# Optimization experiments

Hardware: AMD Instinct MI355X
Metric: run time of the kernel (lower is better)

The kernel has to match this reference:

```python
import jax, jax.numpy as jnp
import numpy as np

N = 20000
NEG_SLOPE = 0.2


def gat_conv(x, src, dst, W, att_src, att_dst, bias, heads, ch, concat):
    # x: [N, F_in]; src/dst: [E] (messages flow src -> dst, softmax grouped by dst)
    n = x.shape[0]
    h = (x @ W).reshape(n, heads, ch)                      # [N, H, C]
    a_s = jnp.sum(h * att_src, axis=-1)                    # [N, H]
    a_d = jnp.sum(h * att_dst, axis=-1)                    # [N, H]
    e = jax.nn.leaky_relu(a_s[src] + a_d[dst], NEG_SLOPE)  # [E, H]
    m = jax.ops.segment_max(e, dst, num_segments=n)        # segment-softmax (stable)
    ex = jnp.exp(e - m[dst])
    denom = jax.ops.segment_sum(ex, dst, num_segments=n)
    alpha = ex / (denom[dst] + 1e-16)                      # [E, H]
    msg = h[src] * alpha[:, :, None]                       # [E, H, C]
    out = jax.ops.segment_sum(msg, dst, num_segments=n)    # [N, H, C]
    out = out.reshape(n, heads * ch) if concat else out.mean(axis=1)
    return out + bias


def setup_inputs() -> dict:
    key = jax.random.key(0)
    ks = jax.random.split(key, 24)
    in_ch, h_ch, out_ch, H, OH = 512, 128, 64, 4, 6
    hid = H * h_ch  # 512
    s = 0.1
    d = {
        "x": jax.random.normal(ks[0], (N, in_ch), jnp.float32),
        "edge_index": jax.random.randint(ks[1], (2, 160000), 0, N, jnp.int32),
        "W1": jax.random.normal(ks[2], (in_ch, H * h_ch), jnp.float32) * s,
        "as1": jax.random.normal(ks[3], (1, H, h_ch), jnp.float32) * s,
        "ad1": jax.random.normal(ks[4], (1, H, h_ch), jnp.float32) * s,
        "b1": jnp.zeros((H * h_ch,), jnp.float32),
        "lW1": jax.random.normal(ks[5], (in_ch, hid), jnp.float32) * s,
        "lb1": jnp.zeros((hid,), jnp.float32),
        "W2": jax.random.normal(ks[6], (hid, H * h_ch), jnp.float32) * s,
        "as2": jax.random.normal(ks[7], (1, H, h_ch), jnp.float32) * s,
        "ad2": jax.random.normal(ks[8], (1, H, h_ch), jnp.float32) * s,
        "b2": jnp.zeros((H * h_ch,), jnp.float32),
        "lW2": jax.random.normal(ks[9], (hid, hid), jnp.float32) * s,
        "lb2": jnp.zeros((hid,), jnp.float32),
        "W3": jax.random.normal(ks[10], (hid, OH * out_ch), jnp.float32) * s,
        "as3": jax.random.normal(ks[11], (1, OH, out_ch), jnp.float32) * s,
        "ad3": jax.random.normal(ks[12], (1, OH, out_ch), jnp.float32) * s,
        "b3": jnp.zeros((out_ch,), jnp.float32),
        "lW3": jax.random.normal(ks[13], (hid, out_ch), jnp.float32) * s,
        "lb3": jnp.zeros((out_ch,), jnp.float32),
    }
    return d


def reference(x, edge_index, W1, as1, ad1, b1, lW1, lb1,
              W2, as2, ad2, b2, lW2, lb2,
              W3, as3, ad3, b3, lW3, lb3):
    n = x.shape[0]
    loops = jnp.arange(n, dtype=edge_index.dtype)  # PyG GATConv add_self_loops=True
    src = jnp.concatenate([edge_index[0], loops])
    dst = jnp.concatenate([edge_index[1], loops])
    h = jax.nn.elu(gat_conv(x, src, dst, W1, as1, ad1, b1, 4, 128, True) + x @ lW1 + lb1)
    h = jax.nn.elu(gat_conv(h, src, dst, W2, as2, ad2, b2, 4, 128, True) + h @ lW2 + lb2)
    out = gat_conv(h, src, dst, W3, as3, ad3, b3, 6, 64, False) + h @ lW3 + lb3
    return out
```

## Files before the change

kernel.cpp:

```cpp
#include <hip/hip_runtime.h>
#include <cstddef>
#include <cstdint>
#include <type_traits>

#define N_NODES 20000
#define NPAD 20096
#define E0_EDGES 160000
#define E_TOT (E0_EDGES + N_NODES)
#define CAP 64

typedef __bf16 bf16x8 __attribute__((ext_vector_type(8)));
typedef float f32x4 __attribute__((ext_vector_type(4)));
typedef ushort ushort8 __attribute__((ext_vector_type(8)));

__device__ __forceinline__ ushort f2bf(float f) {
  uint32_t u = __float_as_uint(f);
  return (ushort)((u + 0x7FFFu + ((u >> 16) & 1u)) >> 16);
}
__device__ __forceinline__ float bf2f(ushort h) {
  return __uint_as_float((uint32_t)h << 16);
}

__device__ __forceinline__ int SW(int r) { return ((r >> 1) & 3) ^ ((r >> 3) & 1); }

#define GLOAD16(g, l)                                                         \
  __builtin_amdgcn_global_load_lds(                                           \
      (const __attribute__((address_space(1))) void*)(uintptr_t)(g),          \
      (__attribute__((address_space(3))) void*)(uint32_t)(uintptr_t)(l),      \
      16, 0, 0)


__global__ void fill_csr_kernel(const int* __restrict__ ei, int* __restrict__ cnt,
                                int* __restrict__ slots) {
  int e = blockIdx.x * blockDim.x + threadIdx.x;
  if (e >= E_TOT) return;
  int src, dst;
  if (e < E0_EDGES) { src = ei[e]; dst = ei[E0_EDGES + e]; }
  else              { src = e - E0_EDGES; dst = src; }
  int pos = atomicAdd(&cnt[dst], 1);
  if (pos < CAP) slots[dst * CAP + pos] = src;
}


__global__ void convert_x_kernel(const float* __restrict__ x, ushort* __restrict__ xb) {
  size_t i = ((size_t)blockIdx.x * blockDim.x + threadIdx.x) * 4;
  if (i >= (size_t)NPAD * 512) return;
  if (i < (size_t)N_NODES * 512) {
    float4 v = *(const float4*)(x + i);
    ushort4 o;
    o.x = f2bf(v.x); o.y = f2bf(v.y); o.z = f2bf(v.z); o.w = f2bf(v.w);
    *(ushort4*)(xb + i) = o;
  } else {
    *(ushort4*)(xb + i) = make_ushort4(0, 0, 0, 0);
  }
}

__global__ void transpose_all_kernel(
    const float* __restrict__ W1, const float* __restrict__ lW1,
    const float* __restrict__ W2, const float* __restrict__ lW2,
    const float* __restrict__ W3, const float* __restrict__ lW3,
    ushort* __restrict__ Bt1, ushort* __restrict__ Bt2, ushort* __restrict__ Bt3) {
  __shared__ float tile[32][33];
  const int K = 512;
  int z = blockIdx.z;
  const float* W; ushort* B; int M;
  switch (z) {
    case 0:  W = W1;  B = Bt1;              M = 512; break;
    case 1:  W = lW1; B = Bt1 + 512 * 512;  M = 512; break;
    case 2:  W = W2;  B = Bt2;              M = 512; break;
    case 3:  W = lW2; B = Bt2 + 512 * 512;  M = 512; break;
    case 4:  W = W3;  B = Bt3;              M = 384; break;
    default: W = lW3; B = Bt3 + 384 * 512;  M = 64;  break;
  }
  int mb = blockIdx.x * 32, kb = blockIdx.y * 32;
  if (mb >= M) return;
  int tx = threadIdx.x, ty = threadIdx.y;
#pragma unroll
  for (int i = 0; i < 32; i += 8)
    tile[ty + i][tx] = W[(size_t)(kb + ty + i) * M + mb + tx];
  __syncthreads();
#pragma unroll
  for (int i = 0; i < 32; i += 8)
    B[(size_t)(mb + ty + i) * K + kb + tx] = f2bf(tile[tx][ty + i]);
}


template <typename Out1T>
__global__ __launch_bounds__(512, 6) void mfma_gemm_kernel(
    const ushort* __restrict__ A,
    const ushort* __restrict__ Bt,
    ushort* __restrict__ out0, int ld0, int split,
    Out1T* __restrict__ out1, int ld1, int Mout1, const float* __restrict__ bias1,
    const float* __restrict__ att_sw, const float* __restrict__ att_dw,
    float* __restrict__ a_sp, float* __restrict__ a_dp,
    int nheads, int headC,
    int NT, int nwg) {
  const int K = 512;
  __shared__ __attribute__((aligned(16))) ushort As[3][128][32];
  __shared__ __attribute__((aligned(16))) ushort Bs[3][128][32];

  int tid = threadIdx.x, lane = tid & 63, wave = tid >> 6;
  int wrow = (wave >> 1) * 32, wcol = (wave & 1) * 64;

  size_t K2 = (size_t)K * 2;
  int rofs = lane >> 2;
  int gch = (lane & 3) ^ SW(rofs);
  int srow = wave * 16;

  int fr = lane & 15, hi = lane >> 4;
  int rch = hi ^ SW(fr);

  char* AsB = (char*)&As[0][0][0];
  char* BsB = (char*)&Bs[0][0][0];

  int q = nwg >> 3, r = nwg & 7;

  for (int w0 = blockIdx.x; w0 < nwg; w0 += gridDim.x) {
    int xcd = w0 & 7, pos = w0 >> 3;
    int wgid = (xcd < r ? xcd * (q + 1) : r * (q + 1) + (xcd - r) * q) + pos;
    int by = wgid / NT, bx = wgid - by * NT;
    int bm = by * 128, bn = bx * 128;

    const char* pA = (const char*)A + (size_t)(bm + srow + rofs) * K2 + gch * 16;
    const char* pB = (const char*)Bt + (size_t)(bn + srow + rofs) * K2 + gch * 16;

    f32x4 acc[2][4] = {};

#pragma unroll
    for (int s = 0; s < 2; ++s) {
      GLOAD16(pA, AsB + s * 8192 + srow * 64);
      GLOAD16(pB, BsB + s * 8192 + srow * 64);
      pA += 64; pB += 64;
    }

    for (int k = 0; k < 16; ++k) {
      if (k + 1 < 16) asm volatile("s_waitcnt vmcnt(2) lgkmcnt(0)" ::: "memory");
      else            asm volatile("s_waitcnt vmcnt(0) lgkmcnt(0)" ::: "memory");
      __builtin_amdgcn_s_barrier();
      asm volatile("" ::: "memory");
      if (k + 2 < 16) {
        int ss = (k + 2) % 3;
        GLOAD16(pA, AsB + ss * 8192 + srow * 64);
        GLOAD16(pB, BsB + ss * 8192 + srow * 64);
        pA += 64; pB += 64;
      }
      {
        int sc = k % 3;
        bf16x8 af[2], bf[4];
#pragma unroll
        for (int i = 0; i < 2; ++i)
          af[i] = *(const bf16x8*)&As[sc][wrow + i * 16 + fr][rch * 8];
#pragma unroll
        for (int j = 0; j < 4; ++j)
          bf[j] = *(const bf16x8*)&Bs[sc][wcol + j * 16 + fr][rch * 8];
#pragma unroll
        for (int i = 0; i < 2; ++i)
#pragma unroll
          for (int j = 0; j < 4; ++j)
            acc[i][j] = __builtin_amdgcn_mfma_f32_16x16x32_bf16(af[i], bf[j], acc[i][j], 0, 0, 0);
      }
      asm volatile("" ::: "memory");
    }

    asm volatile("s_waitcnt lgkmcnt(0)" ::: "memory");
    __builtin_amdgcn_s_barrier();
    asm volatile("" ::: "memory");

    int colg = bn + wcol;
    bool lower = colg < split;
    int g4 = hi << 2;
    int ccol = fr;
#pragma unroll
    for (int i = 0; i < 2; ++i) {
#pragma unroll
      for (int rr = 0; rr < 4; ++rr) {
        int row = bm + wrow + g4 + i * 16 + rr;
        if (row >= N_NODES) continue;
#pragma unroll
        for (int j = 0; j < 4; ++j) {
          int col = colg + j * 16 + ccol;
          float v = acc[i][j][rr];
          if (lower) {
            out0[(size_t)row * ld0 + col] = f2bf(v);
          } else {
            int c1 = col - split;
            if (c1 < Mout1) {
              float b = v + bias1[c1];
              if constexpr (std::is_same<Out1T, ushort>::value)
                out1[(size_t)row * ld1 + c1] = f2bf(b);
              else
                out1[(size_t)row * ld1 + c1] = b;
            }
          }
        }
      }
    }

    if (lower) {
      int hd = colg / headC;
      int cb = colg - hd * headC;
      int half = (cb >> 6) & 1;
      float ws4[4], wd4[4];
#pragma unroll
      for (int j = 0; j < 4; ++j) {
        int cc = hd * headC + cb + j * 16 + ccol;
        ws4[j] = att_sw[cc];
        wd4[j] = att_dw[cc];
      }
#pragma unroll
      for (int i = 0; i < 2; ++i) {
#pragma unroll
        for (int rr = 0; rr < 4; ++rr) {
          float ps = 0.f, pd = 0.f;
#pragma unroll
          for (int j = 0; j < 4; ++j) { ps += acc[i][j][rr] * ws4[j]; pd += acc[i][j][rr] * wd4[j]; }
#pragma unroll
          for (int o = 1; o < 16; o <<= 1) { ps += __shfl_xor(ps, o); pd += __shfl_xor(pd, o); }
          if ((lane & 15) == 0) {
            int row = bm + wrow + g4 + i * 16 + rr;
            if (row < N_NODES) {
              size_t idx = ((size_t)row * nheads + hd) * 2;
              if (headC == 128) {
                a_sp[idx + half] = ps;
                a_dp[idx + half] = pd;
              } else {
                a_sp[idx] = ps;  a_sp[idx + 1] = 0.f;
                a_dp[idx] = pd;  a_dp[idx + 1] = 0.f;
              }
            }
          }
        }
      }
    }
  }
}


template <int H, int C>
__global__ __launch_bounds__(256) void gather12_fused(
    const int* __restrict__ cnt, const int* __restrict__ slots,
    const float* __restrict__ a_sp, const float* __restrict__ a_dp,
    const ushort* __restrict__ hbuf, const float* __restrict__ gat_bias,
    const ushort* __restrict__ skip_in, ushort* __restrict__ outbuf) {
  __shared__ float al[H][CAP];
  __shared__ int srcs[CAP];
  __shared__ float part[4][H * C];
  int n = blockIdx.x;
  int t = threadIdx.x, lane = t & 63, w = t >> 6;
  int deg = min(cnt[n], CAP);

  int sj = 0;
  if (lane < deg) sj = slots[n * CAP + lane];
  {
    int hd = w;
    float e = -1e30f;
    if (lane < deg) {
      size_t is = ((size_t)sj * H + hd) * 2;
      size_t id = ((size_t)n * H + hd) * 2;
      float v = a_sp[is] + a_sp[is + 1] + a_dp[id] + a_dp[id + 1];
      e = v > 0.f ? v : 0.2f * v;
    }
    float m = e;
#pragma unroll
    for (int o = 32; o > 0; o >>= 1) m = fmaxf(m, __shfl_xor(m, o));
    float ex = (lane < deg) ? expf(e - m) : 0.f;
    float s = ex;
#pragma unroll
    for (int o = 32; o > 0; o >>= 1) s += __shfl_xor(s, o);
    float inv = 1.f / (s + 1e-16f);
    if (lane < deg) al[hd][lane] = ex * inv;
  }
  if (w == 0 && lane < deg) srcs[lane] = sj;
  __syncthreads();

  int f0 = 8 * lane, hd = lane >> 4;
  float a8[8] = {};
  for (int j = w; j < deg; j += 4) {
    float a = al[hd][j];
    ushort8 hv = *(const ushort8*)(hbuf + (size_t)srcs[j] * (H * C) + f0);
#pragma unroll
    for (int e = 0; e < 8; ++e) a8[e] += a * bf2f(hv[e]);
  }
  *(f32x4*)&part[w][f0] = *(f32x4*)&a8[0];
  *(f32x4*)&part[w][f0 + 4] = *(f32x4*)&a8[4];
  __syncthreads();

  int g0 = 2 * t;
  float s0 = part[0][g0] + part[1][g0] + part[2][g0] + part[3][g0];
  float s1 = part[0][g0 + 1] + part[1][g0 + 1] + part[2][g0 + 1] + part[3][g0 + 1];
  uint32_t sk = *(const uint32_t*)(skip_in + (size_t)n * (H * C) + g0);
  float o0 = s0 + gat_bias[g0 + 0] + bf2f((ushort)(sk & 0xffffu));
  float o1 = s1 + gat_bias[g0 + 1] + bf2f((ushort)(sk >> 16));
  o0 = o0 > 0.f ? o0 : (expf(o0) - 1.f);
  o1 = o1 > 0.f ? o1 : (expf(o1) - 1.f);
  uint32_t ov = (uint32_t)f2bf(o0) | ((uint32_t)f2bf(o1) << 16);
  *(uint32_t*)(outbuf + (size_t)n * (H * C) + g0) = ov;
}


__global__ __launch_bounds__(128) void gather3_fused(
    const int* __restrict__ cnt, const int* __restrict__ slots,
    const float* __restrict__ a_sp, const float* __restrict__ a_dp,
    const ushort* __restrict__ hbuf , const float* __restrict__ b3,
    float* __restrict__ out ) {
  __shared__ float al[6][CAP];
  __shared__ int srcs[CAP];
  __shared__ float part[6][64];
  int n = blockIdx.x;
  int t = threadIdx.x, lane = t & 63, w = t >> 6;
  int deg = min(cnt[n], CAP);

  int sj = 0;
  if (lane < deg) sj = slots[n * CAP + lane];
#pragma unroll
  for (int hh = 0; hh < 3; ++hh) {
    int hd = 3 * w + hh;
    float e = -1e30f;
    if (lane < deg) {
      size_t is = ((size_t)sj * 6 + hd) * 2;
      size_t id = ((size_t)n * 6 + hd) * 2;
      float v = a_sp[is] + a_sp[is + 1] + a_dp[id] + a_dp[id + 1];
      e = v > 0.f ? v : 0.2f * v;
    }
    float m = e;
#pragma unroll
    for (int o = 32; o > 0; o >>= 1) m = fmaxf(m, __shfl_xor(m, o));
    float ex = (lane < deg) ? expf(e - m) : 0.f;
    float s = ex;
#pragma unroll
    for (int o = 32; o > 0; o >>= 1) s += __shfl_xor(s, o);
    float inv = (1.f / 6.f) / (s + 1e-16f);
    if (lane < deg) al[hd][lane] = ex * inv;
  }
  if (w == 0 && lane < deg) srcs[lane] = sj;
  __syncthreads();

  if (t < 96) {
    int hd = t >> 4, c4 = (t & 15) * 4;
    float a4[4] = {};
    for (int j = 0; j < deg; ++j) {
      float a = al[hd][j];
      ushort4 hv = *(const ushort4*)(hbuf + (size_t)srcs[j] * 384 + hd * 64 + c4);
      a4[0] += a * bf2f(hv.x);
      a4[1] += a * bf2f(hv.y);
      a4[2] += a * bf2f(hv.z);
      a4[3] += a * bf2f(hv.w);
    }
    *(f32x4*)&part[hd][c4] = *(f32x4*)&a4[0];
  }
  __syncthreads();
  if (t < 64) {
    float s = part[0][t] + part[1][t] + part[2][t] +
              part[3][t] + part[4][t] + part[5][t];
    size_t oi = (size_t)n * 64 + t;
    out[oi] += s + b3[t];
  }
}


extern "C" void kernel_launch(void* const* d_in, const int* in_sizes, int n_in,
                              void* d_out, int out_size, void* d_ws, size_t ws_size,
                              hipStream_t stream) {
  const float* x   = (const float*)d_in[0];
  const int*   ei  = (const int*)d_in[1];
  const float* W1  = (const float*)d_in[2];
  const float* as1 = (const float*)d_in[3];
  const float* ad1 = (const float*)d_in[4];
  const float* b1  = (const float*)d_in[5];
  const float* lW1 = (const float*)d_in[6];
  const float* lb1 = (const float*)d_in[7];
  const float* W2  = (const float*)d_in[8];
  const float* as2 = (const float*)d_in[9];
  const float* ad2 = (const float*)d_in[10];
  const float* b2  = (const float*)d_in[11];
  const float* lW2 = (const float*)d_in[12];
  const float* lb2 = (const float*)d_in[13];
  const float* W3  = (const float*)d_in[14];
  const float* as3 = (const float*)d_in[15];
  const float* ad3 = (const float*)d_in[16];
  const float* b3  = (const float*)d_in[17];
  const float* lW3 = (const float*)d_in[18];
  const float* lb3 = (const float*)d_in[19];
  float* out = (float*)d_out;

  char* ws = (char*)d_ws;
  auto alloc = [&](size_t bytes) -> void* {
    void* p = (void*)ws;
    ws += (bytes + 255) & ~(size_t)255;
    return p;
  };
  ushort* xb    = (ushort*)alloc((size_t)NPAD * 512 * 2);
  ushort* Pb    = (ushort*)alloc((size_t)NPAD * 512 * 2);
  ushort* Qb    = (ushort*)alloc((size_t)NPAD * 512 * 2);
  ushort* skipb = (ushort*)alloc((size_t)N_NODES * 512 * 2);
  ushort* hb    = (ushort*)alloc((size_t)N_NODES * 512 * 2);
  ushort* Bt1   = (ushort*)alloc((size_t)1024 * 512 * 2);
  ushort* Bt2   = (ushort*)alloc((size_t)1024 * 512 * 2);
  ushort* Bt3   = (ushort*)alloc((size_t)512 * 512 * 2);
  float*  a_sp  = (float*)alloc((size_t)N_NODES * 6 * 2 * 4);
  float*  a_dp  = (float*)alloc((size_t)N_NODES * 6 * 2 * 4);
  int*    cnt   = (int*)alloc((size_t)N_NODES * 4);
  int*    slots = (int*)alloc((size_t)N_NODES * CAP * 4);

  hipMemsetAsync(cnt, 0, N_NODES * sizeof(int), stream);
  fill_csr_kernel<<<(E_TOT + 255) / 256, 256, 0, stream>>>(ei, cnt, slots);

  convert_x_kernel<<<((NPAD * 512 / 4) + 255) / 256, 256, 0, stream>>>(x, xb);
  transpose_all_kernel<<<dim3(16, 16, 6), dim3(32, 8), 0, stream>>>(
      W1, lW1, W2, lW2, W3, lW3, Bt1, Bt2, Bt3);

  const int NBY = NPAD / 128;
  const int NWG12 = NBY * 8;
  const int NWG3  = NBY * 4;
  const int PERSIST = 256 * 3;
  const int G12 = NWG12 < PERSIST ? NWG12 : PERSIST;
  const int G3  = NWG3  < PERSIST ? NWG3  : PERSIST;

  mfma_gemm_kernel<ushort><<<G12, 512, 0, stream>>>(
      xb, Bt1, hb, 512, 512, skipb, 512, 512, lb1, as1, ad1, a_sp, a_dp, 4, 128,
      8, NWG12);
  gather12_fused<4, 128><<<N_NODES, 256, 0, stream>>>(cnt, slots, a_sp, a_dp, hb, b1, skipb, Pb);

  mfma_gemm_kernel<ushort><<<G12, 512, 0, stream>>>(
      Pb, Bt2, hb, 512, 512, skipb, 512, 512, lb2, as2, ad2, a_sp, a_dp, 4, 128,
      8, NWG12);
  gather12_fused<4, 128><<<N_NODES, 256, 0, stream>>>(cnt, slots, a_sp, a_dp, hb, b2, skipb, Qb);

  mfma_gemm_kernel<float><<<G3, 512, 0, stream>>>(
      Qb, Bt3, hb, 384, 384, out, 64, 64, lb3, as3, ad3, a_sp, a_dp, 6, 64,
      4, NWG3);
  gather3_fused<<<N_NODES, 128, 0, stream>>>(cnt, slots, a_sp, a_dp, hb, b3, out);
}
```

Baseline: 244.9 us.

## Process two nodes per block in gather kernels with software-prefetched neighbor loads

The layer-1/2 and layer-3 gather kernels now handle two destination nodes per 256-thread block, with two waves per node instead of four. This halves the number of blocks. The change also adds a one-step prefetch of the next neighbor row in the aggregation loop, float2 loads for the attention logits, fast __expf, and a 4-wide vectorized epilogue. Each node gets less parallelism across edges, and gather3 now reads srcs[fn][0] unconditionally, even when the node has no neighbors.

```diff
diff --git a/kernel.cpp b/kernel.cpp
--- a/kernel.cpp
+++ b/kernel.cpp
@@ -242,118 +242,149 @@
     const float* __restrict__ a_sp, const float* __restrict__ a_dp,
     const ushort* __restrict__ hbuf, const float* __restrict__ gat_bias,
     const ushort* __restrict__ skip_in, ushort* __restrict__ outbuf) {
-  __shared__ float al[H][CAP];
-  __shared__ int srcs[CAP];
-  __shared__ float part[4][H * C];
-  int n = blockIdx.x;
-  int t = threadIdx.x, lane = t & 63, w = t >> 6;
+  __shared__ float al[2][H][CAP];
+  __shared__ int srcs[2][CAP];
+  __shared__ float part[2][2][H * C];
+  int t = threadIdx.x, lane = t & 63, wave = t >> 6;
+  int nd = wave >> 1, wh = wave & 1;
+  int n = blockIdx.x * 2 + nd;
   int deg = min(cnt[n], CAP);
 
   int sj = 0;
   if (lane < deg) sj = slots[n * CAP + lane];
-  {
-    int hd = w;
+#pragma unroll
+  for (int hh = 0; hh < 2; ++hh) {
+    int hd = 2 * wh + hh;
     float e = -1e30f;
     if (lane < deg) {
-      size_t is = ((size_t)sj * H + hd) * 2;
-      size_t id = ((size_t)n * H + hd) * 2;
-      float v = a_sp[is] + a_sp[is + 1] + a_dp[id] + a_dp[id + 1];
+      float2 s2 = *(const float2*)&a_sp[((size_t)sj * H + hd) * 2];
+      float2 d2 = *(const float2*)&a_dp[((size_t)n * H + hd) * 2];
+      float v = s2.x + s2.y + d2.x + d2.y;
       e = v > 0.f ? v : 0.2f * v;
     }
     float m = e;
 #pragma unroll
     for (int o = 32; o > 0; o >>= 1) m = fmaxf(m, __shfl_xor(m, o));
-    float ex = (lane < deg) ? expf(e - m) : 0.f;
+    float ex = (lane < deg) ? __expf(e - m) : 0.f;
     float s = ex;
 #pragma unroll
     for (int o = 32; o > 0; o >>= 1) s += __shfl_xor(s, o);
     float inv = 1.f / (s + 1e-16f);
-    if (lane < deg) al[hd][lane] = ex * inv;
-  }
-  if (w == 0 && lane < deg) srcs[lane] = sj;
+    if (lane < deg) al[nd][hd][lane] = ex * inv;
+  }
+  if (wh == 0 && lane < deg) srcs[nd][lane] = sj;
   __syncthreads();
 
   int f0 = 8 * lane, hd = lane >> 4;
+  const ushort* hb = hbuf + f0;
   float a8[8] = {};
-  for (int j = w; j < deg; j += 4) {
-    float a = al[hd][j];
-    ushort8 hv = *(const ushort8*)(hbuf + (size_t)srcs[j] * (H * C) + f0);
+  int j = wh;
+  if (j < deg) {
+    ushort8 hv = *(const ushort8*)(hb + (size_t)srcs[nd][j] * (H * C));
+    float a = al[nd][hd][j];
+    for (j += 2; j < deg; j += 2) {
+      ushort8 hv2 = *(const ushort8*)(hb + (size_t)srcs[nd][j] * (H * C));
+      float a2 = al[nd][hd][j];
+#pragma unroll
+      for (int e = 0; e < 8; ++e) a8[e] += a * bf2f(hv[e]);
+      hv = hv2; a = a2;
+    }
 #pragma unroll
     for (int e = 0; e < 8; ++e) a8[e] += a * bf2f(hv[e]);
   }
-  *(f32x4*)&part[w][f0] = *(f32x4*)&a8[0];
-  *(f32x4*)&part[w][f0 + 4] = *(f32x4*)&a8[4];
+  *(f32x4*)&part[nd][wh][f0] = *(f32x4*)&a8[0];
+  *(f32x4*)&part[nd][wh][f0 + 4] = *(f32x4*)&a8[4];
   __syncthreads();
 
-  int g0 = 2 * t;
-  float s0 = part[0][g0] + part[1][g0] + part[2][g0] + part[3][g0];
-  float s1 = part[0][g0 + 1] + part[1][g0 + 1] + part[2][g0 + 1] + part[3][g0 + 1];
-  uint32_t sk = *(const uint32_t*)(skip_in + (size_t)n * (H * C) + g0);
-  float o0 = s0 + gat_bias[g0 + 0] + bf2f((ushort)(sk & 0xffffu));
-  float o1 = s1 + gat_bias[g0 + 1] + bf2f((ushort)(sk >> 16));
-  o0 = o0 > 0.f ? o0 : (expf(o0) - 1.f);
-  o1 = o1 > 0.f ? o1 : (expf(o1) - 1.f);
-  uint32_t ov = (uint32_t)f2bf(o0) | ((uint32_t)f2bf(o1) << 16);
-  *(uint32_t*)(outbuf + (size_t)n * (H * C) + g0) = ov;
-}
-
-
-__global__ __launch_bounds__(128) void gather3_fused(
+  int fn = t >> 7, g0 = (t & 127) * 4;
+  int nn = blockIdx.x * 2 + fn;
+  f32x4 p0 = *(const f32x4*)&part[fn][0][g0];
+  f32x4 p1 = *(const f32x4*)&part[fn][1][g0];
+  float4 bi = *(const float4*)&gat_bias[g0];
+  ushort4 sk = *(const ushort4*)(skip_in + (size_t)nn * (H * C) + g0);
+  float o0 = p0[0] + p1[0] + bi.x + bf2f(sk.x);
+  float o1 = p0[1] + p1[1] + bi.y + bf2f(sk.y);
+  float o2 = p0[2] + p1[2] + bi.z + bf2f(sk.z);
+  float o3 = p0[3] + p1[3] + bi.w + bf2f(sk.w);
+  o0 = o0 > 0.f ? o0 : (__expf(o0) - 1.f);
+  o1 = o1 > 0.f ? o1 : (__expf(o1) - 1.f);
+  o2 = o2 > 0.f ? o2 : (__expf(o2) - 1.f);
+  o3 = o3 > 0.f ? o3 : (__expf(o3) - 1.f);
+  ushort4 ov;
+  ov.x = f2bf(o0); ov.y = f2bf(o1); ov.z = f2bf(o2); ov.w = f2bf(o3);
+  *(ushort4*)(outbuf + (size_t)nn * (H * C) + g0) = ov;
+}
+
+
+__global__ __launch_bounds__(256) void gather3_fused(
     const int* __restrict__ cnt, const int* __restrict__ slots,
     const float* __restrict__ a_sp, const float* __restrict__ a_dp,
     const ushort* __restrict__ hbuf , const float* __restrict__ b3,
     float* __restrict__ out ) {
-  __shared__ float al[6][CAP];
-  __shared__ int srcs[CAP];
-  __shared__ float part[6][64];
-  int n = blockIdx.x;
-  int t = threadIdx.x, lane = t & 63, w = t >> 6;
+  __shared__ float al[2][6][CAP];
+  __shared__ int srcs[2][CAP];
+  __shared__ float part[2][6][64];
+  int t = threadIdx.x, lane = t & 63, wave = t >> 6;
+  int nd = wave >> 1, wh = wave & 1;
+  int n = blockIdx.x * 2 + nd;
   int deg = min(cnt[n], CAP);
 
   int sj = 0;
   if (lane < deg) sj = slots[n * CAP + lane];
 #pragma unroll
   for (int hh = 0; hh < 3; ++hh) {
-    int hd = 3 * w + hh;
+    int hd = 3 * wh + hh;
     float e = -1e30f;
     if (lane < deg) {
-      size_t is = ((size_t)sj * 6 + hd) * 2;
-      size_t id = ((size_t)n * 6 + hd) * 2;
-      float v = a_sp[is] + a_sp[is + 1] + a_dp[id] + a_dp[id + 1];
+      float2 s2 = *(const float2*)&a_sp[((size_t)sj * 6 + hd) * 2];
+      float2 d2 = *(const float2*)&a_dp[((size_t)n * 6 + hd) * 2];
+      float v = s2.x + s2.y + d2.x + d2.y;
       e = v > 0.f ? v : 0.2f * v;
     }
     float m = e;
 #pragma unroll
     for (int o = 32; o > 0; o >>= 1) m = fmaxf(m, __shfl_xor(m, o));
-    float ex = (lane < deg) ? expf(e - m) : 0.f;
+    float ex = (lane < deg) ? __expf(e - m) : 0.f;
     float s = ex;
 #pragma unroll
     for (int o = 32; o > 0; o >>= 1) s += __shfl_xor(s, o);
     float inv = (1.f / 6.f) / (s + 1e-16f);
-    if (lane < deg) al[hd][lane] = ex * inv;
-  }
-  if (w == 0 && lane < deg) srcs[lane] = sj;
+    if (lane < deg) al[nd][hd][lane] = ex * inv;
+  }
+  if (wh == 0 && lane < deg) srcs[nd][lane] = sj;
   __syncthreads();
 
-  if (t < 96) {
-    int hd = t >> 4, c4 = (t & 15) * 4;
+  int tl = t & 127, fn = t >> 7;
+  int nn = blockIdx.x * 2 + fn;
+  int dg = min(cnt[nn], CAP);
+  if (tl < 96) {
+    int hd = tl >> 4, c4 = (tl & 15) * 4;
+    const ushort* hb = hbuf + hd * 64 + c4;
     float a4[4] = {};
-    for (int j = 0; j < deg; ++j) {
-      float a = al[hd][j];
-      ushort4 hv = *(const ushort4*)(hbuf + (size_t)srcs[j] * 384 + hd * 64 + c4);
+    ushort4 hv = *(const ushort4*)(hb + (size_t)srcs[fn][0] * 384);
+    int j = 0;
+    for (; j + 1 < dg; ++j) {
+      ushort4 hv2 = *(const ushort4*)(hb + (size_t)srcs[fn][j + 1] * 384);
+      float a = al[fn][hd][j];
       a4[0] += a * bf2f(hv.x);
       a4[1] += a * bf2f(hv.y);
       a4[2] += a * bf2f(hv.z);
       a4[3] += a * bf2f(hv.w);
-    }
-    *(f32x4*)&part[hd][c4] = *(f32x4*)&a4[0];
+      hv = hv2;
+    }
+    float a = al[fn][hd][j];
+    a4[0] += a * bf2f(hv.x);
+    a4[1] += a * bf2f(hv.y);
+    a4[2] += a * bf2f(hv.z);
+    a4[3] += a * bf2f(hv.w);
+    *(f32x4*)&part[fn][hd][c4] = *(f32x4*)&a4[0];
   }
   __syncthreads();
-  if (t < 64) {
-    float s = part[0][t] + part[1][t] + part[2][t] +
-              part[3][t] + part[4][t] + part[5][t];
-    size_t oi = (size_t)n * 64 + t;
-    out[oi] += s + b3[t];
+  if (tl < 64) {
+    float s = part[fn][0][tl] + part[fn][1][tl] + part[fn][2][tl] +
+              part[fn][3][tl] + part[fn][4][tl] + part[fn][5][tl];
+    size_t oi = (size_t)nn * 64 + tl;
+    out[oi] += s + b3[tl];
   }
 }
 
@@ -416,18 +447,20 @@
   const int G12 = NWG12 < PERSIST ? NWG12 : PERSIST;
   const int G3  = NWG3  < PERSIST ? NWG3  : PERSIST;
 
+  const int NBLK2 = N_NODES / 2;
+
   mfma_gemm_kernel<ushort><<<G12, 512, 0, stream>>>(
       xb, Bt1, hb, 512, 512, skipb, 512, 512, lb1, as1, ad1, a_sp, a_dp, 4, 128,
       8, NWG12);
-  gather12_fused<4, 128><<<N_NODES, 256, 0, stream>>>(cnt, slots, a_sp, a_dp, hb, b1, skipb, Pb);
+  gather12_fused<4, 128><<<NBLK2, 256, 0, stream>>>(cnt, slots, a_sp, a_dp, hb, b1, skipb, Pb);
 
   mfma_gemm_kernel<ushort><<<G12, 512, 0, stream>>>(
       Pb, Bt2, hb, 512, 512, skipb, 512, 512, lb2, as2, ad2, a_sp, a_dp, 4, 128,
       8, NWG12);
-  gather12_fused<4, 128><<<N_NODES, 256, 0, stream>>>(cnt, slots, a_sp, a_dp, hb, b2, skipb, Qb);
+  gather12_fused<4, 128><<<NBLK2, 256, 0, stream>>>(cnt, slots, a_sp, a_dp, hb, b2, skipb, Qb);
 
   mfma_gemm_kernel<float><<<G3, 512, 0, stream>>>(
       Qb, Bt3, hb, 384, 384, out, 64, 64, lb3, as3, ad3, a_sp, a_dp, 6, 64,
       4, NWG3);
-  gather3_fused<<<N_NODES, 128, 0, stream>>>(cnt, slots, a_sp, a_dp, hb, b3, out);
-}
+  gather3_fused<<<NBLK2, 256, 0, stream>>>(cnt, slots, a_sp, a_dp, hb, b3, out);
+}
```

New measurement: 248.9 us. About the same (+1.6%).

## Split layer-1/2 gather into alpha kernel and feature-sliced aggregation kernel

Applied to the files above, without the earlier changes.

The fused per-node gather for layers 1 and 2 is replaced by two kernels. One computes the softmax attention weights per node and head and writes them to a global buffer. The other assigns each block one 64-feature slice and 32 nodes, so consecutive blocks touch different column slices of the hidden buffer and the slice working set fits better in cache. This adds an extra launch and a global round trip for the alpha values per layer. Layer 3's gather also gets a software-prefetched source load, float2 loads and the fast __expf.

```diff
diff --git a/kernel.cpp b/kernel.cpp
--- a/kernel.cpp
+++ b/kernel.cpp
@@ -236,65 +236,88 @@
 }
 
 
-template <int H, int C>
-__global__ __launch_bounds__(256) void gather12_fused(
+template <int H>
+__global__ __launch_bounds__(256) void alpha_kernel(
     const int* __restrict__ cnt, const int* __restrict__ slots,
     const float* __restrict__ a_sp, const float* __restrict__ a_dp,
-    const ushort* __restrict__ hbuf, const float* __restrict__ gat_bias,
-    const ushort* __restrict__ skip_in, ushort* __restrict__ outbuf) {
-  __shared__ float al[H][CAP];
-  __shared__ int srcs[CAP];
-  __shared__ float part[4][H * C];
-  int n = blockIdx.x;
+    float* __restrict__ alf) {
   int t = threadIdx.x, lane = t & 63, w = t >> 6;
+  int n = blockIdx.x * 4 + w;
+  if (n >= N_NODES) return;
   int deg = min(cnt[n], CAP);
-
   int sj = 0;
   if (lane < deg) sj = slots[n * CAP + lane];
-  {
-    int hd = w;
+#pragma unroll
+  for (int hd = 0; hd < H; ++hd) {
     float e = -1e30f;
     if (lane < deg) {
-      size_t is = ((size_t)sj * H + hd) * 2;
-      size_t id = ((size_t)n * H + hd) * 2;
-      float v = a_sp[is] + a_sp[is + 1] + a_dp[id] + a_dp[id + 1];
+      float2 s2 = *(const float2*)&a_sp[((size_t)sj * H + hd) * 2];
+      float2 d2 = *(const float2*)&a_dp[((size_t)n * H + hd) * 2];
+      float v = s2.x + s2.y + d2.x + d2.y;
       e = v > 0.f ? v : 0.2f * v;
     }
     float m = e;
 #pragma unroll
     for (int o = 32; o > 0; o >>= 1) m = fmaxf(m, __shfl_xor(m, o));
-    float ex = (lane < deg) ? expf(e - m) : 0.f;
+    float ex = (lane < deg) ? __expf(e - m) : 0.f;
     float s = ex;
 #pragma unroll
     for (int o = 32; o > 0; o >>= 1) s += __shfl_xor(s, o);
     float inv = 1.f / (s + 1e-16f);
-    if (lane < deg) al[hd][lane] = ex * inv;
-  }
-  if (w == 0 && lane < deg) srcs[lane] = sj;
+    if (lane < deg) alf[((size_t)hd * N_NODES + n) * CAP + lane] = ex * inv;
+  }
+}
+
+
+__global__ __launch_bounds__(256) void gslice12_kernel(
+    const int* __restrict__ cnt, const int* __restrict__ slots,
+    const float* __restrict__ alf, const ushort* __restrict__ hbuf,
+    const float* __restrict__ gat_bias, const ushort* __restrict__ skip_in,
+    ushort* __restrict__ outbuf) {
+  __shared__ float bsh[64];
+  int bid = blockIdx.x;
+  int s = bid & 7, chunk = bid >> 3;
+  int t = threadIdx.x, lane = t & 63, wave = t >> 6;
+  int e8 = lane >> 3, f8 = lane & 7;
+  int soff = s * 64;
+  int hd = s >> 1;
+  const float* alp = alf + (size_t)hd * N_NODES * CAP;
+
+  if (t < 64) bsh[t] = gat_bias[soff + t];
   __syncthreads();
 
-  int f0 = 8 * lane, hd = lane >> 4;
-  float a8[8] = {};
-  for (int j = w; j < deg; j += 4) {
-    float a = al[hd][j];
-    ushort8 hv = *(const ushort8*)(hbuf + (size_t)srcs[j] * (H * C) + f0);
-#pragma unroll
-    for (int e = 0; e < 8; ++e) a8[e] += a * bf2f(hv[e]);
-  }
-  *(f32x4*)&part[w][f0] = *(f32x4*)&a8[0];
-  *(f32x4*)&part[w][f0 + 4] = *(f32x4*)&a8[4];
-  __syncthreads();
-
-  int g0 = 2 * t;
-  float s0 = part[0][g0] + part[1][g0] + part[2][g0] + part[3][g0];
-  float s1 = part[0][g0 + 1] + part[1][g0 + 1] + part[2][g0 + 1] + part[3][g0 + 1];
-  uint32_t sk = *(const uint32_t*)(skip_in + (size_t)n * (H * C) + g0);
-  float o0 = s0 + gat_bias[g0 + 0] + bf2f((ushort)(sk & 0xffffu));
-  float o1 = s1 + gat_bias[g0 + 1] + bf2f((ushort)(sk >> 16));
-  o0 = o0 > 0.f ? o0 : (expf(o0) - 1.f);
-  o1 = o1 > 0.f ? o1 : (expf(o1) - 1.f);
-  uint32_t ov = (uint32_t)f2bf(o0) | ((uint32_t)f2bf(o1) << 16);
-  *(uint32_t*)(outbuf + (size_t)n * (H * C) + g0) = ov;
+#pragma unroll
+  for (int ni = 0; ni < 8; ++ni) {
+    int n = chunk * 32 + wave * 8 + ni;
+    int deg = min(cnt[n], CAP);
+    float acc[8] = {};
+    for (int j0 = 0; j0 < deg; j0 += 8) {
+      int j = j0 + e8;
+      bool v = j < deg;
+      int src = v ? slots[n * CAP + j] : 0;
+      float a = v ? alp[(size_t)n * CAP + j] : 0.f;
+      ushort8 hv = *(const ushort8*)(hbuf + (size_t)src * 512 + soff + f8 * 8);
+#pragma unroll
+      for (int e = 0; e < 8; ++e) acc[e] += a * bf2f(hv[e]);
+    }
+#pragma unroll
+    for (int m = 8; m <= 32; m <<= 1) {
+#pragma unroll
+      for (int e = 0; e < 8; ++e) acc[e] += __shfl_xor(acc[e], m);
+    }
+    if (e8 == 0) {
+      int fb = f8 * 8;
+      ushort8 sk = *(const ushort8*)(skip_in + (size_t)n * 512 + soff + fb);
+      ushort8 ov;
+#pragma unroll
+      for (int e = 0; e < 8; ++e) {
+        float o = acc[e] + bsh[fb + e] + bf2f(sk[e]);
+        o = o > 0.f ? o : (__expf(o) - 1.f);
+        ov[e] = f2bf(o);
+      }
+      *(ushort8*)(outbuf + (size_t)n * 512 + soff + fb) = ov;
+    }
+  }
 }
 
 
@@ -317,19 +340,19 @@
     int hd = 3 * w + hh;
     float e = -1e30f;
     if (lane < deg) {
-      size_t is = ((size_t)sj * 6 + hd) * 2;
-      size_t id = ((size_t)n * 6 + hd) * 2;
-      float v = a_sp[is] + a_sp[is + 1] + a_dp[id] + a_dp[id + 1];
+      float2 s2 = *(const float2*)&a_sp[((size_t)sj * 6 + hd) * 2];
+      float2 d2 = *(const float2*)&a_dp[((size_t)n * 6 + hd) * 2];
+      float v = s2.x + s2.y + d2.x + d2.y;
       e = v > 0.f ? v : 0.2f * v;
     }
     float m = e;
 #pragma unroll
     for (int o = 32; o > 0; o >>= 1) m = fmaxf(m, __shfl_xor(m, o));
-    float ex = (lane < deg) ? expf(e - m) : 0.f;
-    float s = ex;
-#pragma unroll
-    for (int o = 32; o > 0; o >>= 1) s += __shfl_xor(s, o);
-    float inv = (1.f / 6.f) / (s + 1e-16f);
+    float ex = (lane < deg) ? __expf(e - m) : 0.f;
+    float sum = ex;
+#pragma unroll
+    for (int o = 32; o > 0; o >>= 1) sum += __shfl_xor(sum, o);
+    float inv = (1.f / 6.f) / (sum + 1e-16f);
     if (lane < deg) al[hd][lane] = ex * inv;
   }
   if (w == 0 && lane < deg) srcs[lane] = sj;
@@ -337,15 +360,24 @@
 
   if (t < 96) {
     int hd = t >> 4, c4 = (t & 15) * 4;
+    const ushort* hb = hbuf + hd * 64 + c4;
     float a4[4] = {};
-    for (int j = 0; j < deg; ++j) {
+    ushort4 hv = *(const ushort4*)(hb + (size_t)srcs[0] * 384);
+    int j = 0;
+    for (; j + 1 < deg; ++j) {
+      ushort4 hv2 = *(const ushort4*)(hb + (size_t)srcs[j + 1] * 384);
       float a = al[hd][j];
-      ushort4 hv = *(const ushort4*)(hbuf + (size_t)srcs[j] * 384 + hd * 64 + c4);
       a4[0] += a * bf2f(hv.x);
       a4[1] += a * bf2f(hv.y);
       a4[2] += a * bf2f(hv.z);
       a4[3] += a * bf2f(hv.w);
-    }
+      hv = hv2;
+    }
+    float a = al[hd][j];
+    a4[0] += a * bf2f(hv.x);
+    a4[1] += a * bf2f(hv.y);
+    a4[2] += a * bf2f(hv.z);
+    a4[3] += a * bf2f(hv.w);
     *(f32x4*)&part[hd][c4] = *(f32x4*)&a4[0];
   }
   __syncthreads();
@@ -399,6 +431,7 @@
   ushort* Bt3   = (ushort*)alloc((size_t)512 * 512 * 2);
   float*  a_sp  = (float*)alloc((size_t)N_NODES * 6 * 2 * 4);
   float*  a_dp  = (float*)alloc((size_t)N_NODES * 6 * 2 * 4);
+  float*  alf   = (float*)alloc((size_t)4 * N_NODES * CAP * 4);
   int*    cnt   = (int*)alloc((size_t)N_NODES * 4);
   int*    slots = (int*)alloc((size_t)N_NODES * CAP * 4);
 
@@ -416,15 +449,20 @@
   const int G12 = NWG12 < PERSIST ? NWG12 : PERSIST;
   const int G3  = NWG3  < PERSIST ? NWG3  : PERSIST;
 
+  const int GA = N_NODES / 4;
+  const int GS = (N_NODES / 32) * 8;
+
   mfma_gemm_kernel<ushort><<<G12, 512, 0, stream>>>(
       xb, Bt1, hb, 512, 512, skipb, 512, 512, lb1, as1, ad1, a_sp, a_dp, 4, 128,
       8, NWG12);
-  gather12_fused<4, 128><<<N_NODES, 256, 0, stream>>>(cnt, slots, a_sp, a_dp, hb, b1, skipb, Pb);
+  alpha_kernel<4><<<GA, 256, 0, stream>>>(cnt, slots, a_sp, a_dp, alf);
+  gslice12_kernel<<<GS, 256, 0, stream>>>(cnt, slots, alf, hb, b1, skipb, Pb);
 
   mfma_gemm_kernel<ushort><<<G12, 512, 0, stream>>>(
       Pb, Bt2, hb, 512, 512, skipb, 512, 512, lb2, as2, ad2, a_sp, a_dp, 4, 128,
       8, NWG12);
-  gather12_fused<4, 128><<<N_NODES, 256, 0, stream>>>(cnt, slots, a_sp, a_dp, hb, b2, skipb, Qb);
+  alpha_kernel<4><<<GA, 256, 0, stream>>>(cnt, slots, a_sp, a_dp, alf);
+  gslice12_kernel<<<GS, 256, 0, stream>>>(cnt, slots, alf, hb, b2, skipb, Qb);
 
   mfma_gemm_kernel<float><<<G3, 512, 0, stream>>>(
       Qb, Bt3, hb, 384, 384, out, 64, 64, lb3, as3, ad3, a_sp, a_dp, 6, 64,
```

After: 316.0 us. 1.29x slower.
